# Performance work log

Hardware: AMD Instinct MI355X
Metric: run time of the kernel (lower is better)

Reference implementation:

```python
import jax, jax.numpy as jnp
import numpy as np


def _grid_sample_2d(feat, gx, gy):
    """Bilinear grid sample, zeros padding, align_corners=False.
    feat: [B,C,H,W]; gx,gy: [B,S,h,w] normalized coords in [-1,1].
    Returns [B,C,S,h,w]. Matches torch 5D grid_sample with D=1, z=0
    (z pixel coord = (1*1-1)/2 = 0 -> weight 1 on the single depth slice).
    """
    B, C, H, W = feat.shape
    ix = ((gx + 1.0) * W - 1.0) * 0.5  # unnormalize, align_corners=False
    iy = ((gy + 1.0) * H - 1.0) * 0.5
    x0 = jnp.floor(ix)
    y0 = jnp.floor(iy)
    tx = ix - x0  # fractional parts (differentiable w.r.t. grid)
    ty = iy - y0
    x0i = x0.astype(jnp.int32)
    y0i = y0.astype(jnp.int32)
    feat_flat = feat.reshape(B, C, H * W)

    def gather(xi, yi):
        valid = (xi >= 0) & (xi < W) & (yi >= 0) & (yi < H)
        xc = jnp.clip(xi, 0, W - 1)
        yc = jnp.clip(yi, 0, H - 1)
        idx = (yc * W + xc).reshape(B, 1, -1)  # [B,1,S*h*w]
        g = jnp.take_along_axis(feat_flat, idx, axis=2)  # [B,C,S*h*w]
        g = g.reshape(B, C, *xi.shape[1:])  # [B,C,S,h,w]
        return g * valid.astype(feat.dtype)[:, None]

    v00 = gather(x0i, y0i)
    v01 = gather(x0i + 1, y0i)
    v10 = gather(x0i, y0i + 1)
    v11 = gather(x0i + 1, y0i + 1)
    w00 = ((1.0 - tx) * (1.0 - ty))[:, None]
    w01 = (tx * (1.0 - ty))[:, None]
    w10 = ((1.0 - tx) * ty)[:, None]
    w11 = (tx * ty)[:, None]
    return v00 * w00 + v01 * w01 + v10 * w10 + v11 * w11


def setup_inputs() -> dict:
    key = jax.random.key(0)
    k1, k2, k3, k4 = jax.random.split(key, 4)
    B, C, S, H, W = 8, 8, 16, 128, 416
    feat_l = jax.random.normal(k1, (B, C, H, W), dtype=jnp.float32)
    feat_r = jax.random.normal(k2, (B, C, H, W), dtype=jnp.float32)
    # LUT: x,y normalized coords (slightly beyond [-1,1] to exercise zero padding);
    # z channel fixed to 0 exactly as in the module's lut_batch construction.
    lut_xy = jax.random.uniform(k3, (B, S, H, W, 2), dtype=jnp.float32,
                                minval=-1.1, maxval=1.1)
    lut = jnp.concatenate([lut_xy, jnp.zeros((B, S, H, W, 1), jnp.float32)], axis=-1)
    valid_mask = jax.random.bernoulli(k4, 0.8, (B, C, S, H, W))
    return {"feat_l": feat_l, "feat_r": feat_r, "lut": lut,
            "valid_mask": valid_mask, "no_steps": S}


def reference(feat_l, feat_r, lut, valid_mask, no_steps):
    """AnyNet._build_volume_2d: LUT grid_sample warp + masked inf-fill
    + abs-diff + channel-sum cost volume. Returns [B, no_steps, H, W]."""
    gx = lut[..., 0]  # torch grid order: (x, y, z), x indexes width
    gy = lut[..., 1]
    warped = _grid_sample_2d(feat_r, gx, gy)          # [B,C,S,H,W]
    diff = jnp.abs(warped - feat_l[:, :, None])       # broadcast feat_l over S
    cost_disp_feat = jnp.where(valid_mask, diff, jnp.inf)
    cost_volume = jnp.sum(cost_disp_feat, axis=1)     # [B,S,H,W]
    return cost_volume
```

## Files before the change

### kernel.cpp

```cpp
#include <hip/hip_runtime.h>
#include <math.h>

#define BB 8
#define CC 8
#define SS 16
#define HH 128
#define WW 416
#define HWSZ (HH * WW)

typedef unsigned short u16;
typedef unsigned char  u8;

__device__ __forceinline__ float bf2f(u16 v) {
    union { unsigned int u; float f; } x;
    x.u = ((unsigned int)v) << 16;
    return x.f;
}

__device__ __forceinline__ u16 f2bf(float f) {
    union { float ff; unsigned int u; } x;
    x.ff = f;
    unsigned int lsb = (x.u >> 16) & 1u;
    return (u16)((x.u + 0x7FFFu + lsb) >> 16);
}

__global__ __launch_bounds__(256) void anynet_cost_volume(
    const u16* __restrict__ feat_l,
    const u16* __restrict__ feat_r,
    const u16* __restrict__ lut,
    const u8*  __restrict__ vmask,
    u16* __restrict__ out)
{
    const int hw = blockIdx.x * 256 + threadIdx.x;
    const int bs = blockIdx.y;
    const int s  = bs & (SS - 1);
    const int b  = bs >> 4;

    const size_t loff = ((size_t)bs * HWSZ + hw) * 3;
    const float gx = bf2f(lut[loff + 0]);
    const float gy = bf2f(lut[loff + 1]);

    const float ix = ((gx + 1.0f) * (float)WW - 1.0f) * 0.5f;
    const float iy = ((gy + 1.0f) * (float)HH - 1.0f) * 0.5f;
    const float x0f = floorf(ix);
    const float y0f = floorf(iy);
    const float tx = ix - x0f;
    const float ty = iy - y0f;
    const int x0 = (int)x0f;
    const int y0 = (int)y0f;
    const int x1 = x0 + 1;
    const int y1 = y0 + 1;

    const bool vx0 = ((unsigned)x0 < (unsigned)WW);
    const bool vx1 = ((unsigned)x1 < (unsigned)WW);
    const bool vy0 = ((unsigned)y0 < (unsigned)HH);
    const bool vy1 = ((unsigned)y1 < (unsigned)HH);

    const int xc0 = min(max(x0, 0), WW - 1);
    const int xc1 = min(max(x1, 0), WW - 1);
    const int yc0 = min(max(y0, 0), HH - 1);
    const int yc1 = min(max(y1, 0), HH - 1);

    const float w00 = (1.0f - tx) * (1.0f - ty) * ((vx0 && vy0) ? 1.0f : 0.0f);
    const float w01 = tx * (1.0f - ty)          * ((vx1 && vy0) ? 1.0f : 0.0f);
    const float w10 = (1.0f - tx) * ty          * ((vx0 && vy1) ? 1.0f : 0.0f);
    const float w11 = tx * ty                   * ((vx1 && vy1) ? 1.0f : 0.0f);

    const int o00 = yc0 * WW + xc0;
    const int o01 = yc0 * WW + xc1;
    const int o10 = yc1 * WW + xc0;
    const int o11 = yc1 * WW + xc1;

    const u16* __restrict__ fr = feat_r + (size_t)b * CC * HWSZ;
    const u16* __restrict__ fl = feat_l + (size_t)b * CC * HWSZ + hw;
    const u8*  __restrict__ vm = vmask + ((size_t)(b * CC) * SS + s) * HWSZ + hw;

    float acc = 0.0f;
    bool any_invalid = false;
#pragma unroll
    for (int c = 0; c < CC; ++c) {
        const u16* __restrict__ frc = fr + c * HWSZ;
        const float v00 = bf2f(frc[o00]);
        const float v01 = bf2f(frc[o01]);
        const float v10 = bf2f(frc[o10]);
        const float v11 = bf2f(frc[o11]);
        const float warped = v00 * w00 + v01 * w01 + v10 * w10 + v11 * w11;
        const float d = fabsf(warped - bf2f(fl[c * HWSZ]));
        const u8 m = vm[(size_t)c * SS * HWSZ];
        any_invalid |= (m == 0);
        acc += d;
    }

    acc = fminf(fmaxf(acc, 0.0f), 1e30f);
    if (!(acc >= 0.0f && acc <= 1e30f)) acc = 0.0f;
    const u16 ob = any_invalid ? (u16)0x7F7F : f2bf(acc);

    out[(size_t)bs * HWSZ + hw] = ob;
}

extern "C" void kernel_launch(void* const* d_in, const int* in_sizes, int n_in,
                              void* d_out, int out_size, void* d_ws, size_t ws_size,
                              hipStream_t stream) {
    const u16* feat_l = (const u16*)d_in[0];
    const u16* feat_r = (const u16*)d_in[1];
    const u16* lut    = (const u16*)d_in[2];
    const u8*  vmask  = (const u8*)d_in[3];
    u16* out = (u16*)d_out;

    dim3 grid(HWSZ / 256, BB * SS);
    dim3 block(256);
    anynet_cost_volume<<<grid, block, 0, stream>>>(feat_l, feat_r, lut, vmask, out);
}
```

Baseline: 355.4 us.

## Repack features to channel-interleaved layout for 16-byte bilinear gathers

Adds a pre-pass kernel that transposes feat_l and feat_r from planar NCHW into a per-pixel 8-channel packed layout in workspace. The cost-volume kernel then fetches each bilinear corner as a single 16-byte vector load instead of eight scattered 2-byte loads, cutting random gather transactions roughly eightfold. It costs an extra kernel launch and a full read and write of both feature maps each call.

```diff
diff --git a/kernel.cpp b/kernel.cpp
--- a/kernel.cpp
+++ b/kernel.cpp
@@ -10,6 +10,7 @@
 
 typedef unsigned short u16;
 typedef unsigned char  u8;
+typedef unsigned short ushort8 __attribute__((ext_vector_type(8)));
 
 __device__ __forceinline__ float bf2f(u16 v) {
     union { unsigned int u; float f; } x;
@@ -24,9 +25,30 @@
     return (u16)((x.u + 0x7FFFu + lsb) >> 16);
 }
 
-__global__ __launch_bounds__(256) void anynet_cost_volume(
+__global__ __launch_bounds__(256) void pack_feats(
     const u16* __restrict__ feat_l,
     const u16* __restrict__ feat_r,
+    ushort8* __restrict__ pl,
+    ushort8* __restrict__ pr)
+{
+    const int idx = blockIdx.x * 256 + threadIdx.x;
+    const int b = idx / HWSZ;
+    const int p = idx - b * HWSZ;
+    const size_t base = (size_t)b * CC * HWSZ + p;
+
+    ushort8 vr, vl;
+#pragma unroll
+    for (int c = 0; c < CC; ++c) {
+        vr[c] = feat_r[base + (size_t)c * HWSZ];
+        vl[c] = feat_l[base + (size_t)c * HWSZ];
+    }
+    pr[idx] = vr;
+    pl[idx] = vl;
+}
+
+__global__ __launch_bounds__(256) void anynet_cost_volume(
+    const ushort8* __restrict__ pfr,
+    const ushort8* __restrict__ pfl,
     const u16* __restrict__ lut,
     const u8*  __restrict__ vmask,
     u16* __restrict__ out)
@@ -66,36 +88,29 @@
     const float w10 = (1.0f - tx) * ty          * ((vx0 && vy1) ? 1.0f : 0.0f);
     const float w11 = tx * ty                   * ((vx1 && vy1) ? 1.0f : 0.0f);
 
-    const int o00 = yc0 * WW + xc0;
-    const int o01 = yc0 * WW + xc1;
-    const int o10 = yc1 * WW + xc0;
-    const int o11 = yc1 * WW + xc1;
+    const ushort8* __restrict__ frb = pfr + (size_t)b * HWSZ;
+    const ushort8 p00 = frb[yc0 * WW + xc0];
+    const ushort8 p01 = frb[yc0 * WW + xc1];
+    const ushort8 p10 = frb[yc1 * WW + xc0];
+    const ushort8 p11 = frb[yc1 * WW + xc1];
+    const ushort8 fl8 = pfl[(size_t)b * HWSZ + hw];
 
-    const u16* __restrict__ fr = feat_r + (size_t)b * CC * HWSZ;
-    const u16* __restrict__ fl = feat_l + (size_t)b * CC * HWSZ + hw;
-    const u8*  __restrict__ vm = vmask + ((size_t)(b * CC) * SS + s) * HWSZ + hw;
+    const u8* __restrict__ vm = vmask + ((size_t)(b * CC) * SS + s) * HWSZ + hw;
 
     float acc = 0.0f;
     bool any_invalid = false;
 #pragma unroll
     for (int c = 0; c < CC; ++c) {
-        const u16* __restrict__ frc = fr + c * HWSZ;
-        const float v00 = bf2f(frc[o00]);
-        const float v01 = bf2f(frc[o01]);
-        const float v10 = bf2f(frc[o10]);
-        const float v11 = bf2f(frc[o11]);
-        const float warped = v00 * w00 + v01 * w01 + v10 * w10 + v11 * w11;
-        const float d = fabsf(warped - bf2f(fl[c * HWSZ]));
-        const u8 m = vm[(size_t)c * SS * HWSZ];
-        any_invalid |= (m == 0);
+        const float warped = bf2f(p00[c]) * w00 + bf2f(p01[c]) * w01
+                           + bf2f(p10[c]) * w10 + bf2f(p11[c]) * w11;
+        const float d = fabsf(warped - bf2f(fl8[c]));
+        any_invalid |= (vm[(size_t)c * SS * HWSZ] == 0);
         acc += d;
     }
 
     acc = fminf(fmaxf(acc, 0.0f), 1e30f);
     if (!(acc >= 0.0f && acc <= 1e30f)) acc = 0.0f;
-    const u16 ob = any_invalid ? (u16)0x7F7F : f2bf(acc);
-
-    out[(size_t)bs * HWSZ + hw] = ob;
+    out[(size_t)bs * HWSZ + hw] = any_invalid ? (u16)0x7F7F : f2bf(acc);
 }
 
 extern "C" void kernel_launch(void* const* d_in, const int* in_sizes, int n_in,
@@ -107,7 +122,11 @@
     const u8*  vmask  = (const u8*)d_in[3];
     u16* out = (u16*)d_out;
 
+    ushort8* pfr = (ushort8*)d_ws;
+    ushort8* pfl = pfr + (size_t)BB * HWSZ;
+
+    pack_feats<<<dim3(BB * HWSZ / 256), dim3(256), 0, stream>>>(feat_l, feat_r, pfl, pfr);
+
     dim3 grid(HWSZ / 256, BB * SS);
-    dim3 block(256);
-    anynet_cost_volume<<<grid, block, 0, stream>>>(feat_l, feat_r, lut, vmask, out);
+    anynet_cost_volume<<<grid, dim3(256), 0, stream>>>(pfr, pfl, lut, vmask, out);
 }
```

Measured after the change: 342.4 us. -3.7%, faster.
